# Performance work log

Hardware: AMD Instinct MI355X
Metric: run time of the kernel (lower is better)

## Reference

```python
import jax, jax.numpy as jnp
import numpy as np

B, C_IN, C_OUT = 16, 256, 128
V_RAW, N_VERT, K = 10242, 40962, 7


def setup_inputs() -> dict:
    key = jax.random.key(0)
    k1, k2, k3, k4, k5, k6 = jax.random.split(key, 6)
    x = jax.random.normal(k1, (B, C_IN, V_RAW), dtype=jnp.float32)
    W = jax.random.normal(k2, (C_OUT, C_IN), dtype=jnp.float32) * (1.0 / np.sqrt(C_IN))
    b = jax.random.normal(k3, (C_OUT,), dtype=jnp.float32) * 0.01
    up_neigh_indices = jax.random.randint(k4, (N_VERT, K), 0, N_VERT, dtype=jnp.int64)
    down_indices = jax.random.randint(k5, (V_RAW,), 0, N_VERT, dtype=jnp.int64)
    max_pool_indices = jax.random.randint(k6, (B, C_OUT, V_RAW), 0, K, dtype=jnp.int64)
    return {"x": x, "W": W, "b": b,
            "up_neigh_indices": up_neigh_indices,
            "down_indices": down_indices,
            "max_pool_indices": max_pool_indices}


def _feats_indices(n_feats: int, n_raw_vertices: int) -> np.ndarray:
    # torch: floor(linspace(0, n_feats, num=n_raw_vertices*n_feats)); last -= 1
    fi = np.floor(np.linspace(0.0, float(n_feats), num=n_raw_vertices * n_feats))
    fi[-1] -= 1
    return fi.astype(np.int64)


def reference(x, W, b, up_neigh_indices, down_indices, max_pool_indices):
    n_samples, in_feats, n_raw = x.shape
    n_vertices = up_neigh_indices.shape[0]
    out_feats = W.shape[0]

    # per-vertex linear projection: (B, Cin, V) -> (B, Cout, V)
    h = jnp.einsum('bcv,oc->bov', x, W) + b[None, :, None]

    # neighbor table at coarse vertices: (V_raw, K)
    neigh = up_neigh_indices[down_indices]

    # vertices_indices[b, f, v] = neigh[v, max_pool_indices[b, f, v]]
    vi = neigh[jnp.arange(n_raw)[None, None, :], max_pool_indices]  # (B, Cout, V_raw)

    # flatten exactly like torch (row-major over (Cout, V_raw))
    h_flat = h.reshape(n_samples, out_feats * n_raw)
    vi_flat = vi.reshape(n_samples, out_feats * n_raw)
    fi = jnp.asarray(_feats_indices(out_feats, n_raw))  # (Cout*V_raw,) static

    y = jnp.zeros((n_samples, out_feats, n_vertices), dtype=h.dtype)
    y = y.at[jnp.arange(n_samples)[:, None], fi[None, :], vi_flat].set(h_flat)
    return y
```

## Files before the change

### kernel.cpp

```cpp
#include <hip/hip_runtime.h>

#define NB    16
#define CIN   256
#define COUT  128
#define VRAW  10242
#define NVERT 40962
#define QSZ   10241

typedef __attribute__((ext_vector_type(8))) short short8;
typedef __attribute__((ext_vector_type(4))) float floatx4;
typedef float f4u __attribute__((ext_vector_type(4), aligned(4)));

__device__ inline unsigned short f2bf(float f) {
    unsigned u = __builtin_bit_cast(unsigned, f);
    u += 0x7fffu + ((u >> 16) & 1u);
    return (unsigned short)(u >> 16);
}

__global__ __launch_bounds__(256) void convw_kernel(const float* __restrict__ W,
                                                    unsigned short* __restrict__ Wbf) {
    int i = blockIdx.x * 256 + threadIdx.x;
    Wbf[i] = f2bf(W[i]);
}

__global__ __launch_bounds__(256) void prep_kernel(const int* __restrict__ up,
                                                   const int* __restrict__ down,
                                                   unsigned short* __restrict__ T16) {
    int idx = blockIdx.x * 256 + threadIdx.x;
    if (idx >= VRAW * 8) return;
    int v = idx >> 3;
    int k = idx & 7;
    if (k > 6) k = 6;
    T16[idx] = (unsigned short)up[down[v] * 7 + k];
}

#define KC 64
#define VT 128
__global__ __launch_bounds__(256) void gemm_kernel(const float* __restrict__ x,
                                                   const unsigned short* __restrict__ Wbf,
                                                   const float* __restrict__ bias,
                                                   float* __restrict__ h) {
    __shared__ unsigned short xt[VT * KC];
    const int b    = blockIdx.y;
    const int v0   = blockIdx.x * VT;
    const int tid  = threadIdx.x;
    const int wv   = tid >> 6;
    const int lane = tid & 63;
    const int mn   = lane & 15;
    const int q    = lane >> 4;
    const int ow   = (wv & 1) * 64;
    const int vwl  = (wv >> 1) * 64;

    floatx4 acc[4][4];
#pragma unroll
    for (int ot = 0; ot < 4; ot++)
#pragma unroll
        for (int vt = 0; vt < 4; vt++) acc[ot][vt] = (floatx4)0.f;

    for (int c0 = 0; c0 < CIN; c0 += KC) {
#pragma unroll
        for (int i = 0; i < 2; i++) {
            const int tile  = tid + i * 256;
            const int cg    = tile >> 5;
            const int vg    = tile & 31;
            const int vglob = v0 + vg * 4;
            const float* xp = x + ((size_t)b * CIN + c0 + cg * 4) * VRAW + vglob;
            float vals[4][4];
            if (vglob + 3 < VRAW) {
#pragma unroll
                for (int cc = 0; cc < 4; cc++) {
                    f4u rv = *(const f4u*)(xp + (size_t)cc * VRAW);
                    vals[cc][0] = rv.x; vals[cc][1] = rv.y;
                    vals[cc][2] = rv.z; vals[cc][3] = rv.w;
                }
            } else {
#pragma unroll
                for (int cc = 0; cc < 4; cc++)
#pragma unroll
                    for (int jj = 0; jj < 4; jj++)
                        vals[cc][jj] = (vglob + jj < VRAW) ? xp[(size_t)cc * VRAW + jj] : 0.f;
            }
            const int swbase = (cg ^ ((vg & 7) << 1)) << 2;
#pragma unroll
            for (int jj = 0; jj < 4; jj++) {
                const int vloc = vg * 4 + jj;
                unsigned long long pk =
                      (unsigned long long)f2bf(vals[0][jj])
                    | ((unsigned long long)f2bf(vals[1][jj]) << 16)
                    | ((unsigned long long)f2bf(vals[2][jj]) << 32)
                    | ((unsigned long long)f2bf(vals[3][jj]) << 48);
                *(unsigned long long*)&xt[vloc * KC + swbase] = pk;
            }
        }
        __syncthreads();

#pragma unroll
        for (int kk = 0; kk < 2; kk++) {
            short8 bfrag[4];
#pragma unroll
            for (int vt = 0; vt < 4; vt++) {
                const int vloc = vwl + vt * 16 + mn;
                const int cqb  = kk * 8 + q * 2;
                const int cq   = cqb ^ (((vloc >> 2) & 7) << 1);
                bfrag[vt] = *(const short8*)&xt[vloc * KC + (cq << 2)];
            }
#pragma unroll
            for (int ot = 0; ot < 4; ot++) {
                const short8 afrag = *(const short8*)(Wbf + (size_t)(ow + ot * 16 + mn) * CIN
                                                      + c0 + kk * 32 + q * 8);
#pragma unroll
                for (int vt = 0; vt < 4; vt++)
                    acc[ot][vt] = __builtin_amdgcn_mfma_f32_16x16x32_bf16(afrag, bfrag[vt], acc[ot][vt], 0, 0, 0);
            }
        }
        __syncthreads();
    }

#pragma unroll
    for (int ot = 0; ot < 4; ot++) {
#pragma unroll
        for (int r = 0; r < 4; r++) {
            const int o  = ow + ot * 16 + q * 4 + r;
            const float bi = bias[o];
#pragma unroll
            for (int vt = 0; vt < 4; vt++) {
                const int v = v0 + vwl + vt * 16 + mn;
                if (v < VRAW) h[((size_t)b * COUT + o) * VRAW + v] = acc[ot][vt][r] + bi;
            }
        }
    }
}

__global__ __launch_bounds__(1024, 8) void scatter_kernel(const unsigned short* __restrict__ T16,
                                                          const int* __restrict__ mpi,
                                                          const float* __restrict__ h,
                                                          float* __restrict__ y) {
    __shared__ __align__(16) unsigned st[QSZ];
    const int bid = blockIdx.x;
    const int x8  = bid & 7;
    const int j   = bid >> 3;
    const int r   = x8 * 256 + (j >> 2);
    const int qi  = j & 3;
    const int tbase = qi * QSZ;
    const int qlen  = min(QSZ, NVERT - tbase);
    const int tid   = threadIdx.x;

    uint4* st4 = (uint4*)st;
    const uint4 z4 = make_uint4(0u, 0u, 0u, 0u);
    st4[tid] = z4;
    st4[tid + 1024] = z4;
    if (tid < 512) st4[tid + 2048] = z4;
    if (tid == 0) st[10240] = 0u;
    __syncthreads();

    const int* mpiRow = mpi + (size_t)r * VRAW;
#pragma unroll 2
    for (int it = 0; it < 10; it++) {
        const int v = tid + it * 1024;
        const int k = mpiRow[v];
        const uint4 tt = *(const uint4*)(T16 + (size_t)v * 8);
        const unsigned w0 = (k & 2) ? tt.y : tt.x;
        const unsigned w1 = (k & 2) ? tt.w : tt.z;
        const unsigned wsel = (k & 4) ? w1 : w0;
        const unsigned t = (wsel >> ((k & 1) * 16)) & 0xffffu;
        const unsigned lt = t - (unsigned)tbase;
        if (lt < (unsigned)qlen) atomicMax(&st[lt], (unsigned)(v + 1));
    }
    if (tid < 2) {
        const int v = 10240 + tid;
        const int k = mpiRow[v];
        const uint4 tt = *(const uint4*)(T16 + (size_t)v * 8);
        const unsigned w0 = (k & 2) ? tt.y : tt.x;
        const unsigned w1 = (k & 2) ? tt.w : tt.z;
        const unsigned wsel = (k & 4) ? w1 : w0;
        const unsigned t = (wsel >> ((k & 1) * 16)) & 0xffffu;
        const unsigned lt = t - (unsigned)tbase;
        if (lt < (unsigned)qlen) atomicMax(&st[lt], (unsigned)(v + 1));
    }
    __syncthreads();

    const float* hRow = h + (size_t)r * VRAW;
    float* yRow = y + (size_t)r * NVERT + tbase;
#pragma unroll
    for (int i2 = 0; i2 < 2; i2++) {
        const int i = tid + i2 * 1024;
        const uint4 s4 = st4[i];
        f4u out;
        out.x = s4.x ? hRow[s4.x - 1u] : 0.f;
        out.y = s4.y ? hRow[s4.y - 1u] : 0.f;
        out.z = s4.z ? hRow[s4.z - 1u] : 0.f;
        out.w = s4.w ? hRow[s4.w - 1u] : 0.f;
        *(f4u*)(yRow + 4 * i) = out;
    }
    {
        const int i = tid + 2048;
        if (4 * i + 3 < qlen) {
            const uint4 s4 = st4[i];
            f4u out;
            out.x = s4.x ? hRow[s4.x - 1u] : 0.f;
            out.y = s4.y ? hRow[s4.y - 1u] : 0.f;
            out.z = s4.z ? hRow[s4.z - 1u] : 0.f;
            out.w = s4.w ? hRow[s4.w - 1u] : 0.f;
            *(f4u*)(yRow + 4 * i) = out;
        }
    }
    const int base = qlen & ~3;
    if (tid < qlen - base) {
        const int lt = base + tid;
        const unsigned s = st[lt];
        yRow[lt] = s ? hRow[s - 1u] : 0.f;
    }
}

extern "C" void kernel_launch(void* const* d_in, const int* in_sizes, int n_in,
                              void* d_out, int out_size, void* d_ws, size_t ws_size,
                              hipStream_t stream) {
    const float* x    = (const float*)d_in[0];
    const float* W    = (const float*)d_in[1];
    const float* bias = (const float*)d_in[2];
    const int*   up   = (const int*)d_in[3];
    const int*   down = (const int*)d_in[4];
    const int*   mpi  = (const int*)d_in[5];
    float* y = (float*)d_out;

    unsigned short* Wbf = (unsigned short*)d_ws;
    float* h = (float*)((char*)d_ws + 65536);
    unsigned short* T16 = (unsigned short*)((char*)d_ws + 65536 + (size_t)NB * COUT * VRAW * 4);

    convw_kernel<<<COUT * CIN / 256, 256, 0, stream>>>(W, Wbf);
    prep_kernel<<<(VRAW * 8 + 255) / 256, 256, 0, stream>>>(up, down, T16);

    dim3 ggrid((VRAW + VT - 1) / VT, NB);
    gemm_kernel<<<ggrid, 256, 0, stream>>>(x, Wbf, bias, h);

    scatter_kernel<<<NB * COUT * 4, 1024, 0, stream>>>(T16, mpi, h, y);
}
```

Measured before the change: 697.4 us.

## Precompute packed 16-bit scatter targets per row before the scatter kernel

Adds a kernel that resolves each row's max-pool index through the neighbor table once and stores packed 16-bit target vertices, so the four quarter-blocks of the scatter read compact targets instead of re-reading int32 indices and the table. The scatter block size is also reduced to 512 threads with adjusted loops. It costs an extra launch and workspace, and the path only runs if the workspace is large enough.

After: 690.7 us. Within noise of the previous version (-1.0%).

```diff
diff --git a/kernel.cpp b/kernel.cpp
--- a/kernel.cpp
+++ b/kernel.cpp
@@ -6,6 +6,7 @@
 #define VRAW  10242
 #define NVERT 40962
 #define QSZ   10241
+#define NROW  (NB * COUT)
 
 typedef __attribute__((ext_vector_type(8))) short short8;
 typedef __attribute__((ext_vector_type(4))) float floatx4;
@@ -32,6 +33,18 @@
     int k = idx & 7;
     if (k > 6) k = 6;
     T16[idx] = (unsigned short)up[down[v] * 7 + k];
+}
+
+__global__ __launch_bounds__(256) void tgt_kernel(const int* __restrict__ mpi,
+                                                  const unsigned short* __restrict__ T16,
+                                                  unsigned* __restrict__ tgt32) {
+    const int r  = blockIdx.y;
+    const int vp = blockIdx.x * 256 + threadIdx.x;
+    if (vp >= VRAW / 2) return;
+    const int2 kk = *(const int2*)(mpi + (size_t)r * VRAW + 2 * (size_t)vp);
+    const unsigned t0 = T16[(2 * vp)     * 8 + kk.x];
+    const unsigned t1 = T16[(2 * vp + 1) * 8 + kk.y];
+    tgt32[(size_t)r * (VRAW / 2) + vp] = t0 | (t1 << 16);
 }
 
 #define KC 64
@@ -131,10 +144,12 @@
     }
 }
 
-__global__ __launch_bounds__(1024, 8) void scatter_kernel(const unsigned short* __restrict__ T16,
-                                                          const int* __restrict__ mpi,
-                                                          const float* __restrict__ h,
-                                                          float* __restrict__ y) {
+template<int USE_TGT>
+__global__ __launch_bounds__(512, 6) void scatter_kernel(const unsigned* __restrict__ tgt32,
+                                                         const unsigned short* __restrict__ T16,
+                                                         const int* __restrict__ mpi,
+                                                         const float* __restrict__ h,
+                                                         float* __restrict__ y) {
     __shared__ __align__(16) unsigned st[QSZ];
     const int bid = blockIdx.x;
     const int x8  = bid & 7;
@@ -147,43 +162,62 @@
 
     uint4* st4 = (uint4*)st;
     const uint4 z4 = make_uint4(0u, 0u, 0u, 0u);
-    st4[tid] = z4;
-    st4[tid + 1024] = z4;
-    if (tid < 512) st4[tid + 2048] = z4;
+#pragma unroll
+    for (int i = 0; i < 5; i++) st4[tid + i * 512] = z4;
     if (tid == 0) st[10240] = 0u;
     __syncthreads();
 
-    const int* mpiRow = mpi + (size_t)r * VRAW;
-#pragma unroll 2
-    for (int it = 0; it < 10; it++) {
-        const int v = tid + it * 1024;
-        const int k = mpiRow[v];
-        const uint4 tt = *(const uint4*)(T16 + (size_t)v * 8);
-        const unsigned w0 = (k & 2) ? tt.y : tt.x;
-        const unsigned w1 = (k & 2) ? tt.w : tt.z;
-        const unsigned wsel = (k & 4) ? w1 : w0;
-        const unsigned t = (wsel >> ((k & 1) * 16)) & 0xffffu;
-        const unsigned lt = t - (unsigned)tbase;
-        if (lt < (unsigned)qlen) atomicMax(&st[lt], (unsigned)(v + 1));
-    }
-    if (tid < 2) {
-        const int v = 10240 + tid;
-        const int k = mpiRow[v];
-        const uint4 tt = *(const uint4*)(T16 + (size_t)v * 8);
-        const unsigned w0 = (k & 2) ? tt.y : tt.x;
-        const unsigned w1 = (k & 2) ? tt.w : tt.z;
-        const unsigned wsel = (k & 4) ? w1 : w0;
-        const unsigned t = (wsel >> ((k & 1) * 16)) & 0xffffu;
-        const unsigned lt = t - (unsigned)tbase;
-        if (lt < (unsigned)qlen) atomicMax(&st[lt], (unsigned)(v + 1));
+    if (USE_TGT) {
+        const unsigned* tRow = tgt32 + (size_t)r * (VRAW / 2);
+#pragma unroll
+        for (int it = 0; it < 10; it++) {
+            const int vp = tid + it * 512;
+            const unsigned tw = tRow[vp];
+            const unsigned lt0 = (tw & 0xffffu) - (unsigned)tbase;
+            const unsigned lt1 = (tw >> 16)     - (unsigned)tbase;
+            if (lt0 < (unsigned)qlen) atomicMax(&st[lt0], (unsigned)(2 * vp + 1));
+            if (lt1 < (unsigned)qlen) atomicMax(&st[lt1], (unsigned)(2 * vp + 2));
+        }
+        if (tid == 0) {
+            const unsigned tw = tRow[5120];
+            const unsigned lt0 = (tw & 0xffffu) - (unsigned)tbase;
+            const unsigned lt1 = (tw >> 16)     - (unsigned)tbase;
+            if (lt0 < (unsigned)qlen) atomicMax(&st[lt0], 10241u);
+            if (lt1 < (unsigned)qlen) atomicMax(&st[lt1], 10242u);
+        }
+    } else {
+        const int* mpiRow = mpi + (size_t)r * VRAW;
+#pragma unroll 4
+        for (int it = 0; it < 20; it++) {
+            const int v = tid + it * 512;
+            const int k = mpiRow[v];
+            const uint4 tt = *(const uint4*)(T16 + (size_t)v * 8);
+            const unsigned w0 = (k & 2) ? tt.y : tt.x;
+            const unsigned w1 = (k & 2) ? tt.w : tt.z;
+            const unsigned wsel = (k & 4) ? w1 : w0;
+            const unsigned t = (wsel >> ((k & 1) * 16)) & 0xffffu;
+            const unsigned lt = t - (unsigned)tbase;
+            if (lt < (unsigned)qlen) atomicMax(&st[lt], (unsigned)(v + 1));
+        }
+        if (tid < 2) {
+            const int v = 10240 + tid;
+            const int k = mpiRow[v];
+            const uint4 tt = *(const uint4*)(T16 + (size_t)v * 8);
+            const unsigned w0 = (k & 2) ? tt.y : tt.x;
+            const unsigned w1 = (k & 2) ? tt.w : tt.z;
+            const unsigned wsel = (k & 4) ? w1 : w0;
+            const unsigned t = (wsel >> ((k & 1) * 16)) & 0xffffu;
+            const unsigned lt = t - (unsigned)tbase;
+            if (lt < (unsigned)qlen) atomicMax(&st[lt], (unsigned)(v + 1));
+        }
     }
     __syncthreads();
 
     const float* hRow = h + (size_t)r * VRAW;
     float* yRow = y + (size_t)r * NVERT + tbase;
 #pragma unroll
-    for (int i2 = 0; i2 < 2; i2++) {
-        const int i = tid + i2 * 1024;
+    for (int i2 = 0; i2 < 4; i2++) {
+        const int i = tid + i2 * 512;
         const uint4 s4 = st4[i];
         f4u out;
         out.x = s4.x ? hRow[s4.x - 1u] : 0.f;
@@ -223,15 +257,29 @@
     const int*   mpi  = (const int*)d_in[5];
     float* y = (float*)d_out;
 
+    const size_t off_h   = 65536;
+    const size_t off_t16 = off_h + (size_t)NROW * VRAW * 4;
+    const size_t off_tgt = off_t16 + (size_t)VRAW * 8 * 2;
+    const size_t need    = off_tgt + (size_t)NROW * (VRAW / 2) * 4;
+
     unsigned short* Wbf = (unsigned short*)d_ws;
-    float* h = (float*)((char*)d_ws + 65536);
-    unsigned short* T16 = (unsigned short*)((char*)d_ws + 65536 + (size_t)NB * COUT * VRAW * 4);
+    float* h            = (float*)((char*)d_ws + off_h);
+    unsigned short* T16 = (unsigned short*)((char*)d_ws + off_t16);
+    unsigned* tgt32     = (unsigned*)((char*)d_ws + off_tgt);
+    const bool use_tgt  = ws_size >= need;
 
     convw_kernel<<<COUT * CIN / 256, 256, 0, stream>>>(W, Wbf);
     prep_kernel<<<(VRAW * 8 + 255) / 256, 256, 0, stream>>>(up, down, T16);
+    if (use_tgt) {
+        dim3 tgrid((VRAW / 2 + 255) / 256, NROW);
+        tgt_kernel<<<tgrid, 256, 0, stream>>>(mpi, T16, tgt32);
+    }
 
     dim3 ggrid((VRAW + VT - 1) / VT, NB);
     gemm_kernel<<<ggrid, 256, 0, stream>>>(x, Wbf, bias, h);
 
-    scatter_kernel<<<NB * COUT * 4, 1024, 0, stream>>>(T16, mpi, h, y);
-}
+    if (use_tgt)
+        scatter_kernel<1><<<NROW * 4, 512, 0, stream>>>(tgt32, T16, mpi, h, y);
+    else
+        scatter_kernel<0><<<NROW * 4, 512, 0, stream>>>(tgt32, T16, mpi, h, y);
+}
```
